# Performance work log

Measured on AMD Instinct MI355X. Metric: run time of the kernel, lower is better.

## Reference

```python
import jax, jax.numpy as jnp
import numpy as np

D_MODEL = 1024
NUM_HEADS = 16
D_K = D_MODEL // NUM_HEADS


def setup_inputs() -> dict:
    key = jax.random.key(0)
    ks = jax.random.split(key, 11)
    B, S, D = 4, 2048, D_MODEL
    scale = 1.0 / np.sqrt(D)
    return {
        "Q": jax.random.normal(ks[0], (B, S, D), jnp.float32),
        "K": jax.random.normal(ks[1], (B, S, D), jnp.float32),
        "V": jax.random.normal(ks[2], (B, S, D), jnp.float32),
        "Wq": jax.random.normal(ks[3], (D, D), jnp.float32) * scale,
        "bq": jnp.zeros((D,), jnp.float32),
        "Wk": jax.random.normal(ks[4], (D, D), jnp.float32) * scale,
        "bk": jnp.zeros((D,), jnp.float32),
        "Wv": jax.random.normal(ks[5], (D, D), jnp.float32) * scale,
        "bv": jnp.zeros((D,), jnp.float32),
        "Wo": jax.random.normal(ks[6], (D, D), jnp.float32) * scale,
        "bo": jnp.zeros((D,), jnp.float32),
    }


def reference(Q, K, V, Wq, bq, Wk, bk, Wv, bv, Wo, bo):
    B, S, D = Q.shape
    H, Dk = NUM_HEADS, D_K
    # projections: [B,S,D] -> [B,H,S,Dk]
    def proj(x, W, b):
        y = jnp.einsum('bsd,de->bse', x, W.T) + b  # torch Linear: x @ W.T + b
        return y.reshape(B, -1, H, Dk).transpose(0, 2, 1, 3)
    q = proj(Q, Wq, bq)
    k = proj(K, Wk, bk)
    v = proj(V, Wv, bv)
    scores = jnp.einsum('bhqd,bhkd->bhqk', q, k) / np.sqrt(Dk)  # [B,H,S,S]
    attn = jax.nn.softmax(scores, axis=-1)
    out = jnp.einsum('bhqk,bhkd->bhqd', attn, v)  # [B,H,S,Dk]
    out = out.transpose(0, 2, 1, 3).reshape(B, -1, D)
    return jnp.einsum('bsd,de->bse', out, Wo.T) + bo
```

## Files before the change

kernel.cpp:

```cpp
#include <hip/hip_runtime.h>


typedef __bf16 bhalf_t;
typedef __attribute__((ext_vector_type(8)))  __bf16 bf16x8;
typedef __attribute__((ext_vector_type(4)))  __bf16 bf16x4;
typedef __attribute__((ext_vector_type(4)))  float  f32x4;
typedef __attribute__((ext_vector_type(16))) float  f32x16;

typedef __attribute__((address_space(1))) void gvoid_t;
typedef __attribute__((address_space(3))) void lvoid_t;
#define GLD16(g, l) __builtin_amdgcn_global_load_lds((const gvoid_t*)(g), (lvoid_t*)(l), 16, 0, 0)

#define SB0()   __builtin_amdgcn_sched_barrier(0)
#define BARX()  asm volatile("s_barrier" ::: "memory")
#define LGKM0() asm volatile("s_waitcnt lgkmcnt(0)" ::: "memory")
#define VMW(n)  asm volatile("s_waitcnt vmcnt(" #n ")" ::: "memory")

__global__ __launch_bounds__(256) void cvt_all(
    const float* __restrict__ Q, const float* __restrict__ Kin, const float* __restrict__ V,
    const float* __restrict__ Wq, const float* __restrict__ Wk, const float* __restrict__ Wv,
    const float* __restrict__ Wo,
    bhalf_t* __restrict__ Qb, bhalf_t* __restrict__ Kb, bhalf_t* __restrict__ Vb,
    bhalf_t* __restrict__ Wqb, bhalf_t* __restrict__ Wkb, bhalf_t* __restrict__ Wvb,
    bhalf_t* __restrict__ Wob)
{
  size_t t = (size_t)blockIdx.x * 256 + threadIdx.x;
  const float* src; bhalf_t* dst;
  if (t < 2097152)      { src = Q;   dst = Qb; }
  else if (t < 4194304) { src = Kin; dst = Kb; t -= 2097152; }
  else if (t < 6291456) { src = V;   dst = Vb; t -= 4194304; }
  else {
    t -= 6291456;
    int w = (int)(t >> 18); t &= 262143;
    src = (w == 0) ? Wq  : (w == 1) ? Wk  : (w == 2) ? Wv  : Wo;
    dst = (w == 0) ? Wqb : (w == 1) ? Wkb : (w == 2) ? Wvb : Wob;
  }
  float4 f = ((const float4*)src)[t];
  bf16x4 o;
  o.x = (bhalf_t)f.x; o.y = (bhalf_t)f.y; o.z = (bhalf_t)f.z; o.w = (bhalf_t)f.w;
  ((bf16x4*)dst)[t] = o;
}

__device__ __forceinline__ void gemm_core_128(
    const bhalf_t* __restrict__ A, const bhalf_t* __restrict__ B,
    int bm, int bn, bhalf_t* As, bhalf_t* Bs, f32x4 acc[4][4])
{
  const int tid = threadIdx.x, lane = tid & 63, wave = tid >> 6;
  const int wm = wave >> 1, wn = wave & 1;
  const int quad = lane >> 4, tn = lane & 15;
  const int srow = lane >> 2, scol = (lane & 3) * 8;

  const bhalf_t* Ab0 = A + (size_t)(bm * 128 + wave * 16 + srow) * 1024 + scol;
  const bhalf_t* Ab1 = Ab0 + (size_t)64 * 1024;
  const bhalf_t* Bb0 = B + (size_t)(bn * 128 + wave * 16 + srow) * 1024 + scol;
  const bhalf_t* Bb1 = Bb0 + (size_t)64 * 1024;
  bhalf_t* Asw0 = As + wave * 512;  bhalf_t* Asw1 = As + (wave + 4) * 512;
  bhalf_t* Bsw0 = Bs + wave * 512;  bhalf_t* Bsw1 = Bs + (wave + 4) * 512;

  for (int k0 = 0; k0 < 1024; k0 += 32) {
    GLD16(Ab0 + k0, Asw0);
    GLD16(Ab1 + k0, Asw1);
    GLD16(Bb0 + k0, Bsw0);
    GLD16(Bb1 + k0, Bsw1);
    __syncthreads();
    bf16x8 af[4], bfr[4];
#pragma unroll
    for (int i = 0; i < 4; ++i)
      af[i] = *(const bf16x8*)(As + (wm * 64 + i * 16 + tn) * 32 + quad * 8);
#pragma unroll
    for (int j = 0; j < 4; ++j)
      bfr[j] = *(const bf16x8*)(Bs + (wn * 64 + j * 16 + tn) * 32 + quad * 8);
#pragma unroll
    for (int i = 0; i < 4; ++i)
#pragma unroll
      for (int j = 0; j < 4; ++j)
        acc[i][j] = __builtin_amdgcn_mfma_f32_16x16x32_bf16(af[i], bfr[j], acc[i][j], 0, 0, 0);
    __syncthreads();
  }
}

#define PROJ_ITER(T, ISSUE, GATE)                                              \
  {                                                                            \
    bhalf_t* AsB = As + ((T) & 3) * 8192;                                      \
    bhalf_t* BsB = Bs + ((T) & 3) * 8192;                                      \
    bf16x8 af[4], bg[4];                                                       \
    _Pragma("unroll")                                                          \
    for (int i = 0; i < 4; ++i)                                                \
      af[i] = *(const bf16x8*)(AsB + arow + i * 1024 + aswz);                  \
    _Pragma("unroll")                                                          \
    for (int j = 0; j < 4; ++j)                                                \
      bg[j] = *(const bf16x8*)(BsB + brow + j * 1024 + bswz);                  \
    if (ISSUE) {                                                               \
      bhalf_t* And = As + (((T) + 3) & 3) * 8192;                              \
      GLD16(Asrc0 + ((T) + 3) * 32, And + w * 512);                            \
      GLD16(Asrc1 + ((T) + 3) * 32, And + (w + 8) * 512);                      \
    }                                                                          \
    BARX(); LGKM0(); SB0();                                                    \
    __builtin_amdgcn_s_setprio(1);                                             \
    _Pragma("unroll")                                                          \
    for (int i = 0; i < 4; ++i)                                                \
      _Pragma("unroll")                                                        \
      for (int j = 0; j < 4; ++j)                                              \
        acc[i][j] = __builtin_amdgcn_mfma_f32_16x16x32_bf16(af[i], bg[j], acc[i][j], 0, 0, 0); \
    __builtin_amdgcn_s_setprio(0); SB0();                                      \
    BARX();                                                                    \
    _Pragma("unroll")                                                          \
    for (int i = 0; i < 4; ++i)                                                \
      af[i] = *(const bf16x8*)(AsB + arow + (i + 4) * 1024 + aswz);            \
    if (ISSUE) {                                                               \
      bhalf_t* Bnd = Bs + (((T) + 3) & 3) * 8192;                              \
      GLD16(Bsrc0 + ((T) + 3) * 32, Bnd + w * 512);                            \
      GLD16(Bsrc1 + ((T) + 3) * 32, Bnd + (w + 8) * 512);                      \
    }                                                                          \
    BARX(); LGKM0(); SB0();                                                    \
    __builtin_amdgcn_s_setprio(1);                                             \
    _Pragma("unroll")                                                          \
    for (int i = 0; i < 4; ++i)                                                \
      _Pragma("unroll")                                                        \
      for (int j = 0; j < 4; ++j)                                              \
        acc[i + 4][j] = __builtin_amdgcn_mfma_f32_16x16x32_bf16(af[i], bg[j], acc[i + 4][j], 0, 0, 0); \
    __builtin_amdgcn_s_setprio(0); SB0();                                      \
    GATE; SB0();                                                               \
    BARX();                                                                    \
  }

__global__ __launch_bounds__(512, 2) void proj_gemm(
    const bhalf_t* __restrict__ Qb, const bhalf_t* __restrict__ Kb, const bhalf_t* __restrict__ Vb,
    const bhalf_t* __restrict__ Wqb, const bhalf_t* __restrict__ Wkb, const bhalf_t* __restrict__ Wvb,
    const float* __restrict__ bq, const float* __restrict__ bk, const float* __restrict__ bv,
    bhalf_t* __restrict__ qo, bhalf_t* __restrict__ ko, bhalf_t* __restrict__ vto)
{
  __shared__ bhalf_t As[4 * 8192];
  __shared__ bhalf_t Bs[4 * 8192];

  const int bid = blockIdx.x;
  const int wg = (bid & 7) * 48 + (bid >> 3);
  const int seg = wg >> 7;
  const int idx = wg & 127;
  const int bm = idx >> 2, bn = idx & 3;

  const bhalf_t *A, *Bw; const float* bias; bhalf_t* out; float scale; int mode;
  if (seg == 0)      { A = Qb; Bw = Wqb; bias = bq; out = qo;  scale = 0.18033688f; mode = 0; }
  else if (seg == 1) { A = Kb; Bw = Wkb; bias = bk; out = ko;  scale = 1.0f;        mode = 0; }
  else               { A = Vb; Bw = Wvb; bias = bv; out = vto; scale = 1.0f;        mode = 1; }

  const int tid = threadIdx.x, lane = tid & 63, w = tid >> 6;
  const int wm = w >> 2, wn = w & 3;
  const int quad = lane >> 4, tn = lane & 15;

  const int c    = (lane & 7) ^ ((lane >> 3) & 7);
  const int rA   = w * 8 + (lane >> 3);
  const int grow = rA + 128 * (c >> 2);
  const int kcol = (c & 3) * 8;
  const bhalf_t* Asrc0 = A  + (size_t)(bm * 256 + grow) * 1024 + kcol;
  const bhalf_t* Asrc1 = Asrc0 + (size_t)64 * 1024;
  const bhalf_t* Bsrc0 = Bw + (size_t)(bn * 256 + grow) * 1024 + kcol;
  const bhalf_t* Bsrc1 = Bsrc0 + (size_t)64 * 1024;

  const int aswz = (((wm << 2) | quad) ^ (tn & 7)) * 8;
  const int bswz = ((((wn >> 1) << 2) | quad) ^ (tn & 7)) * 8;
  const int arow = tn * 64;
  const int brow = (((wn & 1) << 6) + tn) * 64;

  f32x4 acc[8][4];
#pragma unroll
  for (int i = 0; i < 8; ++i)
#pragma unroll
    for (int j = 0; j < 4; ++j)
      acc[i][j] = (f32x4){0.f, 0.f, 0.f, 0.f};

#pragma unroll
  for (int t = 0; t < 3; ++t) {
    bhalf_t* And = As + t * 8192;
    bhalf_t* Bnd = Bs + t * 8192;
    GLD16(Asrc0 + t * 32, And + w * 512);
    GLD16(Asrc1 + t * 32, And + (w + 8) * 512);
    GLD16(Bsrc0 + t * 32, Bnd + w * 512);
    GLD16(Bsrc1 + t * 32, Bnd + (w + 8) * 512);
  }
  VMW(8); SB0();
  BARX();

#pragma unroll 4
  for (int t = 0; t < 28; ++t) PROJ_ITER(t, true, VMW(8));
  PROJ_ITER(28, true,  VMW(8));
  PROJ_ITER(29, false, VMW(4));
  PROJ_ITER(30, false, VMW(0));
  PROJ_ITER(31, false, (void)0);

#pragma unroll
  for (int i = 0; i < 8; ++i)
#pragma unroll
    for (int j = 0; j < 4; ++j) {
      const int n = bn * 256 + wn * 64 + j * 16 + tn;
      const float bsv = bias[n];
      const int h = n >> 6, dk = n & 63;
#pragma unroll
      for (int r = 0; r < 4; ++r) {
        const int m = bm * 256 + wm * 128 + i * 16 + quad * 4 + r;
        const int b = m >> 11, s = m & 2047;
        const float v = (acc[i][j][r] + bsv) * scale;
        size_t addr;
        if (mode == 0) addr = (((size_t)(b * 16 + h)) * 2048 + s) * 64 + dk;
        else {
          const int s2 = (s & ~12) | ((s & 4) << 1) | ((s & 8) >> 1);
          addr = (((size_t)(b * 16 + h)) * 64 + dk) * 2048 + s2;
        }
        out[addr] = (bhalf_t)v;
      }
    }
}

__global__ __launch_bounds__(256) void out_gemm(
    const bhalf_t* __restrict__ A, const bhalf_t* __restrict__ Bw,
    const float* __restrict__ bias, float* __restrict__ Cout)
{
  __shared__ bhalf_t As[4096];
  __shared__ bhalf_t Bs[4096];
  const int bm = blockIdx.x & 63, bn = blockIdx.x >> 6;

  f32x4 acc[4][4];
#pragma unroll
  for (int i = 0; i < 4; ++i)
#pragma unroll
    for (int j = 0; j < 4; ++j)
      acc[i][j] = (f32x4){0.f, 0.f, 0.f, 0.f};

  gemm_core_128(A, Bw, bm, bn, As, Bs, acc);

  const int lane = threadIdx.x & 63, wave = threadIdx.x >> 6;
  const int wm = wave >> 1, wn = wave & 1, quad = lane >> 4, tn = lane & 15;
#pragma unroll
  for (int i = 0; i < 4; ++i)
#pragma unroll
    for (int j = 0; j < 4; ++j) {
      const int n = bn * 128 + wn * 64 + j * 16 + tn;
      const float bsv = bias[n];
#pragma unroll
      for (int r = 0; r < 4; ++r) {
        const int m = bm * 128 + wm * 64 + i * 16 + quad * 4 + r;
        Cout[(size_t)m * 1024 + n] = acc[i][j][r] + bsv;
      }
    }
}

__global__ __launch_bounds__(256, 2) void attn_kernel(
    const bhalf_t* __restrict__ qp, const bhalf_t* __restrict__ kp,
    const bhalf_t* __restrict__ vtp, bhalf_t* __restrict__ outp)
{
  __shared__ bhalf_t Klds[4096];
  __shared__ bhalf_t Vtlds[4096];

  const int tid = threadIdx.x, lane = tid & 63, wave = tid >> 6;
  const int q31 = lane & 31, h = lane >> 5;
  const int bh = blockIdx.y, qt = blockIdx.x;

  const bhalf_t* qbase = qp + (((size_t)bh * 2048) + qt * 256 + wave * 64 + q31) * 64;
  bf16x8 qf[2][4];
#pragma unroll
  for (int qs = 0; qs < 2; ++qs)
#pragma unroll
    for (int ks = 0; ks < 4; ++ks)
      qf[qs][ks] = *(const bf16x8*)(qbase + qs * 32 * 64 + ks * 16 + h * 8);

  f32x16 Ot[2][2];
#pragma unroll
  for (int qs = 0; qs < 2; ++qs)
#pragma unroll
    for (int dd = 0; dd < 2; ++dd)
#pragma unroll
      for (int i = 0; i < 16; ++i) Ot[qs][dd][i] = 0.f;
  float Lp[2] = {0.f, 0.f};

  const bhalf_t* kbase  = kp  + (size_t)bh * 2048 * 64;
  const bhalf_t* vtbase = vtp + (size_t)bh * 64 * 2048;

  const int rloc = lane >> 3;
  const int cg8  = ((lane & 7) ^ rloc) * 8;
  const int q7 = q31 & 7;

  for (int kv0 = 0; kv0 < 2048; kv0 += 64) {
#pragma unroll
    for (int i = 0; i < 2; ++i) {
      const int r0 = (wave * 2 + i) * 8;
      GLD16(kbase + (size_t)(kv0 + r0 + rloc) * 64 + cg8, Klds + r0 * 64);
      GLD16(vtbase + (size_t)(r0 + rloc) * 2048 + kv0 + cg8, Vtlds + r0 * 64);
    }
    __syncthreads();

    bf16x8 pb[2][4];
#pragma unroll
    for (int mb = 0; mb < 2; ++mb) {
      bf16x8 ka[4];
#pragma unroll
      for (int ks = 0; ks < 4; ++ks)
        ka[ks] = *(const bf16x8*)(Klds + (mb * 32 + q31) * 64 + ((2 * ks + h) ^ q7) * 8);
#pragma unroll
      for (int qs = 0; qs < 2; ++qs) {
        f32x16 S;
#pragma unroll
        for (int i = 0; i < 16; ++i) S[i] = 0.f;
#pragma unroll
        for (int ks = 0; ks < 4; ++ks)
          S = __builtin_amdgcn_mfma_f32_32x32x16_bf16(ka[ks], qf[qs][ks], S, 0, 0, 0);
        float ls = 0.f;
#pragma unroll
        for (int half = 0; half < 2; ++half) {
          bf16x8 pk;
#pragma unroll
          for (int j = 0; j < 8; ++j) {
            const float e = __builtin_amdgcn_exp2f(S[half * 8 + j]);
            ls += e;
            pk[j] = (bhalf_t)e;
          }
          pb[qs][mb * 2 + half] = pk;
        }
        Lp[qs] += ls;
      }
    }

#pragma unroll
    for (int dd = 0; dd < 2; ++dd)
#pragma unroll
      for (int kb = 0; kb < 4; ++kb) {
        const bf16x8 va = *(const bf16x8*)(Vtlds + (dd * 32 + q31) * 64 + ((2 * kb + h) ^ q7) * 8);
#pragma unroll
        for (int qs = 0; qs < 2; ++qs)
          Ot[qs][dd] = __builtin_amdgcn_mfma_f32_32x32x16_bf16(va, pb[qs][kb], Ot[qs][dd], 0, 0, 0);
      }
    __syncthreads();
  }

  const int b = bh >> 4, hh = bh & 15;
#pragma unroll
  for (int qs = 0; qs < 2; ++qs) {
    const float Lt = Lp[qs] + __shfl_xor(Lp[qs], 32, 64);
    const float linv = 1.0f / Lt;
    const int s = qt * 256 + wave * 64 + qs * 32 + q31;
    bhalf_t* ob = outp + ((size_t)(b * 2048 + s)) * 1024 + hh * 64;
#pragma unroll
    for (int dd = 0; dd < 2; ++dd)
#pragma unroll
      for (int g = 0; g < 4; ++g) {
        bf16x4 o;
        o.x = (bhalf_t)(Ot[qs][dd][4 * g + 0] * linv);
        o.y = (bhalf_t)(Ot[qs][dd][4 * g + 1] * linv);
        o.z = (bhalf_t)(Ot[qs][dd][4 * g + 2] * linv);
        o.w = (bhalf_t)(Ot[qs][dd][4 * g + 3] * linv);
        *(bf16x4*)(ob + dd * 32 + g * 8 + h * 4) = o;
      }
  }
}

extern "C" void kernel_launch(void* const* d_in, const int* in_sizes, int n_in,
                              void* d_out, int out_size, void* d_ws, size_t ws_size,
                              hipStream_t stream)
{
  const float* Q  = (const float*)d_in[0];
  const float* K  = (const float*)d_in[1];
  const float* V  = (const float*)d_in[2];
  const float* Wq = (const float*)d_in[3];
  const float* bq = (const float*)d_in[4];
  const float* Wk = (const float*)d_in[5];
  const float* bk = (const float*)d_in[6];
  const float* Wv = (const float*)d_in[7];
  const float* bv = (const float*)d_in[8];
  const float* Wo = (const float*)d_in[9];
  const float* bo = (const float*)d_in[10];

  char* ws = (char*)d_ws;
  const size_t SZ = 8192ull * 1024 * 2;
  const size_t WZ = 1024ull * 1024 * 2;
  bhalf_t* Qb   = (bhalf_t*)(ws);
  bhalf_t* Kb   = (bhalf_t*)(ws + SZ);
  bhalf_t* Vb   = (bhalf_t*)(ws + 2 * SZ);
  bhalf_t* Wqb  = (bhalf_t*)(ws + 3 * SZ);
  bhalf_t* Wkb  = (bhalf_t*)(ws + 3 * SZ + WZ);
  bhalf_t* Wvb  = (bhalf_t*)(ws + 3 * SZ + 2 * WZ);
  bhalf_t* Wob  = (bhalf_t*)(ws + 3 * SZ + 3 * WZ);
  bhalf_t* q_p  = (bhalf_t*)(ws + 3 * SZ + 4 * WZ);
  bhalf_t* k_p  = (bhalf_t*)(ws + 4 * SZ + 4 * WZ);
  bhalf_t* vt_p = (bhalf_t*)(ws + 5 * SZ + 4 * WZ);
  bhalf_t* attn_o = Qb;

  cvt_all<<<28672, 256, 0, stream>>>(Q, K, V, Wq, Wk, Wv, Wo,
                                     Qb, Kb, Vb, Wqb, Wkb, Wvb, Wob);
  proj_gemm<<<384, 512, 0, stream>>>(Qb, Kb, Vb, Wqb, Wkb, Wvb,
                                     bq, bk, bv, q_p, k_p, vt_p);
  attn_kernel<<<dim3(8, 64), 256, 0, stream>>>(q_p, k_p, vt_p, attn_o);
  out_gemm<<<512, 256, 0, stream>>>(attn_o, Wob, bo, (float*)d_out);
}
```

Baseline: 366.3 us.

## Software-pipeline LDS fragment loads in the projection GEMM and cut barriers

New measurement: 375.5 us. 1.03x slower.

```diff
diff --git a/kernel.cpp b/kernel.cpp
--- a/kernel.cpp
+++ b/kernel.cpp
@@ -13,7 +13,6 @@
 
 #define SB0()   __builtin_amdgcn_sched_barrier(0)
 #define BARX()  asm volatile("s_barrier" ::: "memory")
-#define LGKM0() asm volatile("s_waitcnt lgkmcnt(0)" ::: "memory")
 #define VMW(n)  asm volatile("s_waitcnt vmcnt(" #n ")" ::: "memory")
 
 __global__ __launch_bounds__(256) void cvt_all(
@@ -79,49 +78,58 @@
   }
 }
 
-#define PROJ_ITER(T, ISSUE, GATE)                                              \
+#define PH1(T, BG, ISSUE)                                                      \
   {                                                                            \
-    bhalf_t* AsB = As + ((T) & 3) * 8192;                                      \
-    bhalf_t* BsB = Bs + ((T) & 3) * 8192;                                      \
-    bf16x8 af[4], bg[4];                                                       \
-    _Pragma("unroll")                                                          \
-    for (int i = 0; i < 4; ++i)                                                \
-      af[i] = *(const bf16x8*)(AsB + arow + i * 1024 + aswz);                  \
-    _Pragma("unroll")                                                          \
-    for (int j = 0; j < 4; ++j)                                                \
-      bg[j] = *(const bf16x8*)(BsB + brow + j * 1024 + bswz);                  \
     if (ISSUE) {                                                               \
       bhalf_t* And = As + (((T) + 3) & 3) * 8192;                              \
       GLD16(Asrc0 + ((T) + 3) * 32, And + w * 512);                            \
       GLD16(Asrc1 + ((T) + 3) * 32, And + (w + 8) * 512);                      \
     }                                                                          \
-    BARX(); LGKM0(); SB0();                                                    \
+    {                                                                          \
+      bhalf_t* AsB = As + ((T) & 3) * 8192;                                    \
+      _Pragma("unroll")                                                        \
+      for (int i = 0; i < 4; ++i)                                              \
+        afB[i] = *(const bf16x8*)(AsB + arow + (i + 4) * 1024 + aswz);         \
+    }                                                                          \
+    SB0();                                                                     \
     __builtin_amdgcn_s_setprio(1);                                             \
     _Pragma("unroll")                                                          \
     for (int i = 0; i < 4; ++i)                                                \
       _Pragma("unroll")                                                        \
       for (int j = 0; j < 4; ++j)                                              \
-        acc[i][j] = __builtin_amdgcn_mfma_f32_16x16x32_bf16(af[i], bg[j], acc[i][j], 0, 0, 0); \
-    __builtin_amdgcn_s_setprio(0); SB0();                                      \
-    BARX();                                                                    \
-    _Pragma("unroll")                                                          \
-    for (int i = 0; i < 4; ++i)                                                \
-      af[i] = *(const bf16x8*)(AsB + arow + (i + 4) * 1024 + aswz);            \
+        acc[i][j] = __builtin_amdgcn_mfma_f32_16x16x32_bf16(afA[i], BG[j], acc[i][j], 0, 0, 0); \
+    __builtin_amdgcn_s_setprio(0);                                             \
+    SB0();                                                                     \
+  }
+
+#define PH2(T, BG, BGN, ISSUE, PRIME, GATE, DOBAR)                             \
+  {                                                                            \
     if (ISSUE) {                                                               \
       bhalf_t* Bnd = Bs + (((T) + 3) & 3) * 8192;                              \
       GLD16(Bsrc0 + ((T) + 3) * 32, Bnd + w * 512);                            \
       GLD16(Bsrc1 + ((T) + 3) * 32, Bnd + (w + 8) * 512);                      \
     }                                                                          \
-    BARX(); LGKM0(); SB0();                                                    \
+    if (PRIME) {                                                               \
+      bhalf_t* AsN = As + (((T) + 1) & 3) * 8192;                              \
+      bhalf_t* BsN = Bs + (((T) + 1) & 3) * 8192;                              \
+      _Pragma("unroll")                                                        \
+      for (int i = 0; i < 4; ++i)                                              \
+        afA[i] = *(const bf16x8*)(AsN + arow + i * 1024 + aswz);               \
+      _Pragma("unroll")                                                        \
+      for (int j = 0; j < 4; ++j)                                              \
+        BGN[j] = *(const bf16x8*)(BsN + brow + j * 1024 + bswz);               \
+    }                                                                          \
+    SB0();                                                                     \
     __builtin_amdgcn_s_setprio(1);                                             \
     _Pragma("unroll")                                                          \
     for (int i = 0; i < 4; ++i)                                                \
       _Pragma("unroll")                                                        \
       for (int j = 0; j < 4; ++j)                                              \
-        acc[i + 4][j] = __builtin_amdgcn_mfma_f32_16x16x32_bf16(af[i], bg[j], acc[i + 4][j], 0, 0, 0); \
-    __builtin_amdgcn_s_setprio(0); SB0();                                      \
-    GATE; SB0();                                                               \
-    BARX();                                                                    \
+        acc[i + 4][j] = __builtin_amdgcn_mfma_f32_16x16x32_bf16(afB[i], BG[j], acc[i + 4][j], 0, 0, 0); \
+    __builtin_amdgcn_s_setprio(0);                                             \
+    SB0();                                                                     \
+    GATE;                                                                      \
+    if (DOBAR) BARX();                                                         \
   }
 
 __global__ __launch_bounds__(512, 2) void proj_gemm(
@@ -169,6 +177,8 @@
     for (int j = 0; j < 4; ++j)
       acc[i][j] = (f32x4){0.f, 0.f, 0.f, 0.f};
 
+  bf16x8 afA[4], afB[4], bg0[4], bg1[4];
+
 #pragma unroll
   for (int t = 0; t < 3; ++t) {
     bhalf_t* And = As + t * 8192;
@@ -178,15 +188,30 @@
     GLD16(Bsrc0 + t * 32, Bnd + w * 512);
     GLD16(Bsrc1 + t * 32, Bnd + (w + 8) * 512);
   }
-  VMW(8); SB0();
+  VMW(4); SB0();
   BARX();
-
-#pragma unroll 4
-  for (int t = 0; t < 28; ++t) PROJ_ITER(t, true, VMW(8));
-  PROJ_ITER(28, true,  VMW(8));
-  PROJ_ITER(29, false, VMW(4));
-  PROJ_ITER(30, false, VMW(0));
-  PROJ_ITER(31, false, (void)0);
+#pragma unroll
+  for (int i = 0; i < 4; ++i)
+    afA[i] = *(const bf16x8*)(As + arow + i * 1024 + aswz);
+#pragma unroll
+  for (int j = 0; j < 4; ++j)
+    bg0[j] = *(const bf16x8*)(Bs + brow + j * 1024 + bswz);
+
+#pragma unroll 1
+  for (int t = 0; t < 28; t += 2) {
+    PH1(t, bg0, true);
+    PH2(t, bg0, bg1, true, true, VMW(4), true);
+    PH1(t + 1, bg1, true);
+    PH2(t + 1, bg1, bg0, true, true, VMW(4), true);
+  }
+  PH1(28, bg0, true);
+  PH2(28, bg0, bg1, true, true, VMW(4), true);
+  PH1(29, bg1, false);
+  PH2(29, bg1, bg0, false, true, VMW(0), true);
+  PH1(30, bg0, false);
+  PH2(30, bg0, bg1, false, true, (void)0, true);
+  PH1(31, bg1, false);
+  PH2(31, bg1, bg0, false, false, (void)0, false);
 
 #pragma unroll
   for (int i = 0; i < 8; ++i)
```
